# Kernel optimization log

Measured on AMD Instinct MI355X. Metric: run time of the kernel, lower is better.

The kernel has to match this reference:

```python
import jax, jax.numpy as jnp
import numpy as np

B, C, H, W = 4, 96, 256, 256
HEADS = 4
WH = WW = 8            # window size
QKV_D = C // HEADS     # qkv_dim defaults to in_channels // num_heads
N = WH * WW            # tokens per window
EPS = 1e-6


def _rel_index():
    # Swin-style relative position index, [N, N], constant
    coords = np.stack(np.meshgrid(np.arange(WH), np.arange(WW), indexing='ij'), 0).reshape(2, -1)
    rel = coords[:, :, None] - coords[:, None, :]
    rel[0] += WH - 1
    rel[1] += WW - 1
    return rel[0] * (2 * WW - 1) + rel[1]

REL = jnp.asarray(_rel_index())  # int32 [N, N]


def setup_inputs() -> dict:
    key = jax.random.key(0)
    ks = jax.random.split(key, 8)
    s = lambda k, shape: jax.random.normal(k, shape, jnp.float32) * 0.02
    return dict(
        x=jax.random.normal(ks[0], (B, C, H, W), jnp.float32),
        norm_w=jnp.ones((C,), jnp.float32),                      # RMSNorm inside MHA (channel-last tokens)
        qkv_w=s(ks[1], (3 * HEADS * QKV_D, C)),
        qkv_b=jnp.zeros((3 * HEADS * QKV_D,), jnp.float32),
        proj_w=s(ks[2], (C, HEADS * QKV_D)),
        proj_b=jnp.zeros((C,), jnp.float32),
        bias_table=s(ks[3], ((2 * WH - 1) * (2 * WW - 1),)),     # WindowScoreBias table (shared across heads)
        mlp_norm_w=jnp.ones((1, C, 1, 1), jnp.float32),          # RMSNorm1((1,C,1,1), dim=1)
        w1_w=s(ks[4], (2 * C, C, 1, 1)),                         # mid = out_channels*mlp_ratio = 2C
        w1_b=jnp.zeros((2 * C,), jnp.float32),
        w2_w=s(ks[5], (C, C, 3, 3)),                             # mid//2 = C -> C, 3x3
        w2_b=jnp.zeros((C,), jnp.float32),
    )


def rms_norm(x, w, axis):
    v = jnp.mean(x * x, axis=axis, keepdims=True)
    return x * jax.lax.rsqrt(v + EPS) * w


def conv2d(x, w, b):
    y = jax.lax.conv_general_dilated(x, w, (1, 1), 'VALID',
                                     dimension_numbers=('NCHW', 'OIHW', 'NCHW'))
    return y + b[None, :, None, None]


def reference(x, norm_w, qkv_w, qkv_b, proj_w, proj_b, bias_table,
              mlp_norm_w, w1_w, w1_b, w2_w, w2_b):
    B_, C_, H_, W_ = x.shape
    nH, nW = H_ // WH, W_ // WW
    # ---- windowed MHA with norm fused in and relative bias ----
    # window partition: [B,C,H,W] -> [B*nWin, N, C]
    xw = x.reshape(B_, C_, nH, WH, nW, WW).transpose(0, 2, 4, 3, 5, 1).reshape(-1, N, C_)
    xn = rms_norm(xw, norm_w, -1)
    qkv = xn @ qkv_w.T + qkv_b                                  # [Bn, N, 3*h*d]
    qkv = qkv.reshape(-1, N, 3, HEADS, QKV_D).transpose(2, 0, 3, 1, 4)  # [3, Bn, h, N, d]
    q, k, v = qkv[0], qkv[1], qkv[2]
    bias = bias_table[REL]                                      # [N, N], broadcast over batch/heads
    scores = jnp.einsum('bhnd,bhmd->bhnm', q, k) / jnp.sqrt(jnp.float32(QKV_D)) + bias
    attn = jax.nn.softmax(scores, axis=-1)
    o = jnp.einsum('bhnm,bhmd->bhnd', attn, v)
    o = o.transpose(0, 2, 1, 3).reshape(-1, N, HEADS * QKV_D)
    o = o @ proj_w.T + proj_b
    # reverse window partition
    o = o.reshape(B_, nH, nW, WH, WW, C_).transpose(0, 5, 1, 3, 2, 4).reshape(B_, C_, H_, W_)
    x = x + o
    # ---- GLU conv MLP residual ----
    y = rms_norm(x, mlp_norm_w, 1)
    y = conv2d(y, w1_w, w1_b)                                   # 1x1, C -> 2C
    a, g = jnp.split(y, 2, axis=1)
    y = a * jax.nn.sigmoid(g)                                   # GLU along channels
    # ReplicationPad2dDetach: edge pad whose padded ring carries no gradient
    yp = jnp.pad(jax.lax.stop_gradient(y), ((0, 0), (0, 0), (1, 1), (1, 1)), mode='edge')
    yp = yp.at[:, :, 1:-1, 1:-1].set(y)
    y = conv2d(yp, w2_w, w2_b)                                  # 3x3 valid on padded -> same size
    y = jnp.where(y >= 0, y, 0.1 * y)                           # leaky_relu(0.1)
    return x + y
```

## Files before the change

kernel.cpp:

```cpp
#include <hip/hip_runtime.h>
#include <hip/hip_bf16.h>

#define CC 96

typedef short short8  __attribute__((ext_vector_type(8)));
typedef short short4v __attribute__((ext_vector_type(4)));
typedef float f32x4   __attribute__((ext_vector_type(4)));
typedef _Float16 half4 __attribute__((ext_vector_type(4)));

#if __has_builtin(__builtin_amdgcn_mfma_f32_16x16x16_f16)
  #define MFMA16(a,b,c) __builtin_amdgcn_mfma_f32_16x16x16_f16((a),(b),(c),0,0,0)
#else
  #define MFMA16(a,b,c) __builtin_amdgcn_mfma_f32_16x16x16f16((a),(b),(c),0,0,0)
#endif

static __device__ __forceinline__ ushort f2bf(float f) {
  __hip_bfloat16 h = __float2bfloat16(f);
  return *reinterpret_cast<ushort*>(&h);
}
static __device__ __forceinline__ float bf2f(ushort u) {
  union { unsigned int u; float f; } v; v.u = ((unsigned int)u) << 16; return v.f;
}

#define QSCALE 0.20412414523193154f

__global__ void prep_kernel(const float* __restrict__ qkv_w,
                            const float* __restrict__ qkv_b,
                            const float* __restrict__ proj_w,
                            const float* __restrict__ w2w,
                            const float* __restrict__ w1w,
                            __hip_bfloat16* __restrict__ qkvp,
                            float* __restrict__ qkvb2,
                            __hip_bfloat16* __restrict__ projp,
                            __hip_bfloat16* __restrict__ w2p,
                            __hip_bfloat16* __restrict__ w1p,
                            __hip_bfloat16* __restrict__ vwp)
{
  const int i = blockIdx.x*256 + threadIdx.x;
  if (i < 36864) {
    const int e = i & 7, lane = (i >> 3) & 63;
    const int rest = i >> 9;
    const int mt = rest % 6, r2 = rest / 6;
    const int ks = r2 % 3, h = r2 / 3;
    const int od = mt*16 + (lane & 15);
    const int sec = od >> 5, d = od & 31;
    const int c = ks*32 + (lane >> 4)*8 + e;
    float val = 0.f;
    if (d < 24) {
      val = qkv_w[(sec*96 + h*24 + d)*96 + c];
      if (sec == 0) val *= QSCALE;
    }
    qkvp[i] = __float2bfloat16(val);
  }
  const int jb = i - 36864;
  if (jb >= 0 && jb < 384) {
    const int h = jb / 96, od = jb - h*96;
    const int sec = od >> 5, d = od & 31;
    float val = 0.f;
    if (d < 24) {
      val = qkv_b[sec*96 + h*24 + d];
      if (sec == 0) val *= QSCALE;
    }
    qkvb2[jb] = val;
  }
  const int j = i - 37248;
  if (j >= 0 && j < 9216) {
    const int e = j & 7, lane = (j >> 3) & 63;
    const int rest = j >> 9;
    const int nt = rest % 6, ks = rest / 6;
    const int oc = nt*16 + (lane & 15);
    const int dd = ks*32 + (lane >> 4)*8 + e;
    projp[j] = __float2bfloat16(proj_w[oc*96 + dd]);
  }
  const int k = i - 46464;
  if (k >= 0 && k < 82944) {
    const int e = k & 7;
    const int lane = (k >> 3) & 63;
    const int rest = k >> 9;
    const int nf = rest % 6;
    const int r2 = rest / 6;
    const int kc = r2 % 3;
    const int tap = r2 / 3;
    const int cidx = kc*32 + (lane >> 4)*8 + e;
    const int oc = nf*16 + (lane & 15);
    const int ky = tap / 3, kx = tap - ky*3;
    w2p[k] = __float2bfloat16(w2w[((oc*96 + cidx)*3 + ky)*3 + kx]);
  }
  const int m = i - 129408;
  if (m >= 0 && m < 18432) {
    const int e = m & 7, lane = (m >> 3) & 63;
    const int rest = m >> 9;
    const int nt = rest % 12, ks = rest / 12;
    const int oc = nt*16 + (lane & 15);
    const int c  = ks*32 + (lane >> 4)*8 + e;
    w1p[m] = __float2bfloat16(w1w[oc*96 + c]);
  }
  const int v = i - 147840;
  if (v >= 0 && v < 12288) {
    const int e = v & 7, lane = (v >> 3) & 63;
    const int rest = v >> 9;
    const int nt2 = rest % 2, r2 = rest / 2;
    const int ks = r2 % 3, h = r2 / 3;
    const int d = nt2*16 + (lane & 15);
    const int c = ks*32 + (lane >> 4)*8 + e;
    const float val = (d < 24) ? qkv_w[(192 + h*24 + d)*96 + c] : 0.f;
    vwp[v] = __float2bfloat16(val);
  }
}

__global__ __launch_bounds__(512, 2) void attn_kernel(
    const float* __restrict__ x,
    const float* __restrict__ norm_w,
    const __hip_bfloat16* __restrict__ qkvp,
    const float* __restrict__ qkvb2,
    const __hip_bfloat16* __restrict__ vwp,
    const __hip_bfloat16* __restrict__ projp,
    const float* __restrict__ proj_b,
    const float* __restrict__ bias_table,
    float* __restrict__ out)
{
  extern __shared__ char smem[];
  ushort* xn   = (ushort*)smem;
  ushort* xr   = (ushort*)(smem + 26624);
  float*  btab = (float*)(smem + 51200);

  const int wp = blockIdx.x;
  const int b   = wp >> 9;
  const int wy  = (wp >> 4) & 31;
  const int wxp = wp & 15;
  const int t  = threadIdx.x;
  const int y0 = wy*8, x0 = wxp*16;
  const int l  = t & 63;
  const int W  = __builtin_amdgcn_readfirstlane(t >> 6);
  const int w2 = W >> 2, h = W & 3;
  const int lr = l & 15, g = l >> 4;

  for (int i = t; i < 225; i += 512) btab[i] = bias_table[i];

  {
    const int p = t >> 2, q = t & 3;
    const int ty = p >> 4, tx = p & 15;
    const float* xp = x + (size_t)(b*CC + q*24)*65536 + (size_t)(y0+ty)*256 + x0 + tx;
    float xv[24]; float ss = 0.f;
    #pragma unroll
    for (int i = 0; i < 24; i++) { xv[i] = xp[(size_t)i*65536]; ss += xv[i]*xv[i]; }
    ss += __shfl_xor(ss, 1);
    ss += __shfl_xor(ss, 2);
    const float s = rsqrtf(ss * (1.f/96.f) + 1e-6f);
    const int row = (tx >> 3)*64 + ty*8 + (tx & 7);
    #pragma unroll
    for (int k2 = 0; k2 < 3; k2++) {
      short8 pk, pr;
      #pragma unroll
      for (int q2 = 0; q2 < 8; q2++) {
        pr[q2] = (short)f2bf(xv[k2*8+q2]);
        pk[q2] = (short)f2bf(xv[k2*8+q2] * s * norm_w[q*24 + k2*8 + q2]);
      }
      *(short8*)(xn + row*104 + q*24 + k2*8) = pk;
      *(short8*)(xr + row*96  + q*24 + k2*8) = pr;
    }
  }
  __syncthreads();

  half4 qf[2][4], kf[2][4];
  #pragma unroll
  for (int pass = 0; pass < 2; pass++) {
    f32x4 acc[2][4];
    #pragma unroll
    for (int m2 = 0; m2 < 2; m2++)
      #pragma unroll
      for (int nt = 0; nt < 4; nt++) acc[m2][nt] = (f32x4)0.f;
    #pragma unroll
    for (int ks = 0; ks < 3; ks++) {
      short8 bfr[4];
      #pragma unroll
      for (int nt = 0; nt < 4; nt++)
        bfr[nt] = *(const short8*)((const char*)xn + (w2*64 + nt*16 + lr)*208 + g*16 + ks*64);
      #pragma unroll
      for (int m2 = 0; m2 < 2; m2++) {
        const short8 afr = *(const short8*)(qkvp + ((h*3+ks)*6 + pass*2 + m2)*512 + l*8);
        #pragma unroll
        for (int nt = 0; nt < 4; nt++)
          acc[m2][nt] = __builtin_amdgcn_mfma_f32_16x16x32_bf16(afr, bfr[nt], acc[m2][nt], 0, 0, 0);
      }
    }
    #pragma unroll
    for (int m2 = 0; m2 < 2; m2++) {
      const f32x4 bb = *(const f32x4*)(qkvb2 + h*96 + (pass*2+m2)*16 + g*4);
      #pragma unroll
      for (int nt = 0; nt < 4; nt++)
        #pragma unroll
        for (int r = 0; r < 4; r++) {
          const float v = acc[m2][nt][r] + bb[r];
          if (pass == 0) qf[m2][nt][r] = (_Float16)v;
          else           kf[m2][nt][r] = (_Float16)v;
        }
    }
  }

  half4 pa[4][4];
  #pragma unroll
  for (int qt = 0; qt < 4; qt++) {
    f32x4 sacc[4];
    #pragma unroll
    for (int kt = 0; kt < 4; kt++) {
      f32x4 s0 = MFMA16(kf[0][kt], qf[0][qt], (f32x4)0.f);
      sacc[kt] = MFMA16(kf[1][kt], qf[1][qt], s0);
    }
    const int q = qt*16 + lr;
    const int aq = (q >> 3)*15 + (q & 7);
    float vv[4][4];
    float mx = -1e30f;
    #pragma unroll
    for (int kt = 0; kt < 4; kt++)
      #pragma unroll
      for (int r = 0; r < 4; r++) {
        const int k = kt*16 + g*4 + r;
        vv[kt][r] = sacc[kt][r] + btab[aq + 112 - ((k >> 3)*15 + (k & 7))];
        mx = fmaxf(mx, vv[kt][r]);
      }
    mx = fmaxf(mx, __shfl_xor(mx, 16));
    mx = fmaxf(mx, __shfl_xor(mx, 32));
    float sum = 0.f;
    #pragma unroll
    for (int kt = 0; kt < 4; kt++)
      #pragma unroll
      for (int r = 0; r < 4; r++) { vv[kt][r] = __expf(vv[kt][r] - mx); sum += vv[kt][r]; }
    sum += __shfl_xor(sum, 16);
    sum += __shfl_xor(sum, 32);
    const float rinv = 1.f / sum;
    #pragma unroll
    for (int kt = 0; kt < 4; kt++)
      #pragma unroll
      for (int r = 0; r < 4; r++) pa[kt][qt][r] = (_Float16)(vv[kt][r] * rinv);
  }

  half4 vb[4][2];
  {
    f32x4 vacc[4][2];
    #pragma unroll
    for (int kt = 0; kt < 4; kt++) { vacc[kt][0] = (f32x4)0.f; vacc[kt][1] = (f32x4)0.f; }
    #pragma unroll
    for (int ks = 0; ks < 3; ks++) {
      short8 afr[4];
      #pragma unroll
      for (int kt = 0; kt < 4; kt++)
        afr[kt] = *(const short8*)((const char*)xn + (w2*64 + kt*16 + lr)*208 + g*16 + ks*64);
      #pragma unroll
      for (int nt2 = 0; nt2 < 2; nt2++) {
        const short8 vwf = *(const short8*)(vwp + ((h*3+ks)*2+nt2)*512 + l*8);
        #pragma unroll
        for (int kt = 0; kt < 4; kt++)
          vacc[kt][nt2] = __builtin_amdgcn_mfma_f32_16x16x32_bf16(afr[kt], vwf, vacc[kt][nt2], 0, 0, 0);
      }
    }
    #pragma unroll
    for (int nt2 = 0; nt2 < 2; nt2++) {
      const float vbias = qkvb2[h*96 + 64 + nt2*16 + lr];
      #pragma unroll
      for (int kt = 0; kt < 4; kt++)
        #pragma unroll
        for (int r = 0; r < 4; r++)
          vb[kt][nt2][r] = (_Float16)(vacc[kt][nt2][r] + vbias);
    }
  }

  f32x4 oacc[4][2];
  #pragma unroll
  for (int qt = 0; qt < 4; qt++) { oacc[qt][0] = (f32x4)0.f; oacc[qt][1] = (f32x4)0.f; }
  #pragma unroll
  for (int kt = 0; kt < 4; kt++)
    #pragma unroll
    for (int qt = 0; qt < 4; qt++) {
      oacc[qt][0] = MFMA16(pa[kt][qt], vb[kt][0], oacc[qt][0]);
      oacc[qt][1] = MFMA16(pa[kt][qt], vb[kt][1], oacc[qt][1]);
    }
  __syncthreads();

  #pragma unroll
  for (int qt = 0; qt < 4; qt++)
    #pragma unroll
    for (int r = 0; r < 4; r++) {
      const int row = w2*64 + qt*16 + g*4 + r;
      xn[row*104 + h*24 + lr] = f2bf(oacc[qt][0][r]);
      if (lr < 8) xn[row*104 + h*24 + 16 + lr] = f2bf(oacc[qt][1][r]);
    }
  __syncthreads();

  {
    f32x4 pacc[6];
    #pragma unroll
    for (int nt = 0; nt < 6; nt++) pacc[nt] = (f32x4)0.f;
    #pragma unroll
    for (int ks = 0; ks < 3; ks++) {
      const short8 af = *(const short8*)((const char*)xn + (lr + W*16)*208 + g*16 + ks*64);
      #pragma unroll
      for (int nt = 0; nt < 6; nt++) {
        const short8 bf = *(const short8*)(projp + (ks*6+nt)*512 + l*8);
        pacc[nt] = __builtin_amdgcn_mfma_f32_16x16x32_bf16(af, bf, pacc[nt], 0, 0, 0);
      }
    }
    __syncthreads();
    ushort* oT = xn;
    #pragma unroll
    for (int nt = 0; nt < 6; nt++) {
      const int oc = lr + nt*16;
      const float bias = proj_b[oc];
      short4v pk;
      #pragma unroll
      for (int r = 0; r < 4; r++) {
        const int row = W*16 + g*4 + r;
        pk[r] = (short)f2bf(pacc[nt][r] + bias + bf2f(xr[row*96 + oc]));
      }
      *(short4v*)((char*)oT + oc*264 + (g*4 + W*16)*2) = pk;
    }
  }
  __syncthreads();

  {
    const ushort* oT = xn;
    #pragma unroll
    for (int k2 = 0; k2 < 6; k2++) {
      const int e = t + k2*512;
      const int oc = e >> 5, q5 = e & 31;
      const int ty = q5 >> 2, tq = q5 & 3;
      const int m = (tq >> 1)*64 + ty*8 + (tq & 1)*4;
      const short4v ov = *(const short4v*)((const char*)oT + oc*264 + m*2);
      const size_t gidx = (size_t)(b*CC+oc)*65536 + (size_t)(y0+ty)*256 + x0 + tq*4;
      float4 res;
      res.x = bf2f((ushort)ov[0]);
      res.y = bf2f((ushort)ov[1]);
      res.z = bf2f((ushort)ov[2]);
      res.w = bf2f((ushort)ov[3]);
      *(float4*)(out + gidx) = res;
    }
  }
}

__global__ __launch_bounds__(256, 2) void mlp1_kernel(
    const float* __restrict__ x1,
    const float* __restrict__ mlp_norm_w,
    const __hip_bfloat16* __restrict__ w1p,
    const float* __restrict__ w1_b,
    __hip_bfloat16* __restrict__ y)
{
  __shared__ ushort xn[128*104];
  const int blk = blockIdx.x;
  const int b   = blk >> 9;
  const int p0  = (blk & 511) << 7;
  const int t   = threadIdx.x;
  const int l   = t & 63;
  const int w   = __builtin_amdgcn_readfirstlane(t >> 6);
  const int lr  = l & 15, g = l >> 4;

  {
    const int p = t >> 1, half = t & 1;
    const float* xp = x1 + (size_t)(b*CC + half*48)*65536 + p0 + p;
    float xv[48];
    float ss = 0.f;
    #pragma unroll
    for (int i = 0; i < 48; i++) { xv[i] = xp[(size_t)i*65536]; ss += xv[i]*xv[i]; }
    ss += __shfl_xor(ss, 1);
    const float s = rsqrtf(ss*(1.f/96.f) + 1e-6f);
    #pragma unroll
    for (int i = 0; i < 48; i += 2) {
      const int c = half*48 + i;
      union { ushort u[2]; uint v; } pk;
      pk.u[0] = f2bf(xv[i]   * s * mlp_norm_w[c]);
      pk.u[1] = f2bf(xv[i+1] * s * mlp_norm_w[c+1]);
      *(uint*)(&xn[p*104 + c]) = pk.v;
    }
  }

  f32x4 acc[2][12];
  #pragma unroll
  for (int m2 = 0; m2 < 2; m2++)
    #pragma unroll
    for (int nt = 0; nt < 12; nt++) acc[m2][nt] = (f32x4)0.f;

  #pragma unroll
  for (int ks = 0; ks < 3; ks++) {
    short8 afr[2];
    #pragma unroll
    for (int m2 = 0; m2 < 2; m2++)
      afr[m2] = *(const short8*)((const char*)xn + (lr + (w*2+m2)*16)*208 + g*16 + ks*64);
    #pragma unroll
    for (int nt = 0; nt < 12; nt++) {
      const short8 bfr = *(const short8*)(w1p + ((ks*12+nt)*64 + l)*8);
      #pragma unroll
      for (int m2 = 0; m2 < 2; m2++)
        acc[m2][nt] = __builtin_amdgcn_mfma_f32_16x16x32_bf16(afr[m2], bfr, acc[m2][nt], 0, 0, 0);
    }
  }

  #pragma unroll
  for (int m2 = 0; m2 < 2; m2++)
    #pragma unroll
    for (int nt = 0; nt < 6; nt++) {
      const int oc = nt*16 + lr;
      const float ab = w1_b[oc], gb = w1_b[96+oc];
      #pragma unroll
      for (int r = 0; r < 4; r++) {
        const int row = (w*2+m2)*16 + g*4 + r;
        const float a  = acc[m2][nt][r]   + ab;
        const float gg = acc[m2][nt+6][r] + gb;
        xn[row*104 + oc] = f2bf(a / (1.f + __expf(-gg)));
      }
    }
  __syncthreads();

  __hip_bfloat16* yp = y + ((size_t)(b*65536 + p0))*96;
  #pragma unroll
  for (int k2 = 0; k2 < 6; k2++) {
    const int e = t + k2*256;
    const int p = e / 12, ch = e - p*12;
    const short8 v = *(const short8*)(&xn[p*104 + ch*8]);
    *(short8*)((ushort*)yp + p*96 + ch*8) = v;
  }
}

__global__ __launch_bounds__(256) void conv3_kernel(
    const __hip_bfloat16* __restrict__ y,
    const __hip_bfloat16* __restrict__ w2p,
    const float* __restrict__ w2_b,
    float* __restrict__ xout)
{
  extern __shared__ char smem[];
  ushort* A = (ushort*)smem;
  float*  O = (float*)smem;

  const int vbid = (blockIdx.x & 7)*256 + (blockIdx.x >> 3);
  const int b   = vbid >> 9;
  const int rem = vbid & 511;
  const int ch  = rem >> 7;
  const int rp  = rem & 127;
  const int px0 = ch << 6;
  const int t   = threadIdx.x;
  const int w   = __builtin_amdgcn_readfirstlane(t >> 6);
  const int l   = t & 63;
  const int m15 = l & 15, lh = l >> 4;

  for (int e = t; e < 3168; e += 256) {
    const int seg  = e / 12;
    const int part = e - seg*12;
    const int ky = seg / 66;
    const int px = seg - ky*66;
    const int gy = min(255, max(0, 2*rp + ky - 1));
    const int gx = min(255, max(0, px0 + px - 1));
    const short8 v = *(const short8*)(y + ((size_t)(b*65536 + gy*256 + gx))*96 + part*8);
    *(short8*)(A + seg*104 + part*8) = v;
  }

  f32x4 resid[12];
  #pragma unroll
  for (int k2 = 0; k2 < 12; k2++) {
    const int e = t + k2*256;
    const int oc = e >> 5;
    const int j  = (e & 31) * 4;
    const int gy = 2*rp + (j >> 6);
    const int px = px0 + (j & 63);
    resid[k2] = *(const f32x4*)(xout + ((size_t)(b*CC + oc))*65536 + (size_t)gy*256 + px);
  }
  __syncthreads();

  f32x4 acc0[6], acc1[6];
  #pragma unroll
  for (int nf = 0; nf < 6; ++nf) { acc0[nf] = (f32x4)0.f; acc1[nf] = (f32x4)0.f; }

  for (int tap = 0; tap < 9; ++tap) {
    const int ky = tap / 3, kx = tap - ky*3;
    for (int kc = 0; kc < 3; ++kc) {
      const int cb = kc*32 + lh*8;
      const short8 a0 = *(const short8*)(A + ((ky  )*66 + 16*w + m15 + kx)*104 + cb);
      const short8 a1 = *(const short8*)(A + ((ky+1)*66 + 16*w + m15 + kx)*104 + cb);
      const short8* bp = (const short8*)w2p + ((size_t)(tap*3 + kc)*6)*64 + l;
      #pragma unroll
      for (int nf = 0; nf < 6; ++nf) {
        const short8 bf = bp[nf*64];
        acc0[nf] = __builtin_amdgcn_mfma_f32_16x16x32_bf16(a0, bf, acc0[nf], 0, 0, 0);
        acc1[nf] = __builtin_amdgcn_mfma_f32_16x16x32_bf16(a1, bf, acc1[nf], 0, 0, 0);
      }
    }
  }
  __syncthreads();

  {
    const int jb = 16*w + lh*4;
    #pragma unroll
    for (int nf = 0; nf < 6; ++nf) {
      const int oc = nf*16 + m15;
      *(f32x4*)(O + oc*132 + jb)      = acc0[nf];
      *(f32x4*)(O + oc*132 + 64 + jb) = acc1[nf];
    }
  }
  __syncthreads();

  #pragma unroll
  for (int k2 = 0; k2 < 12; ++k2) {
    const int e = t + k2*256;
    const int oc = e >> 5;
    const int j  = (e & 31) * 4;
    f32x4 v = *(const f32x4*)(O + oc*132 + j);
    const float bb = w2_b[oc];
    const int gy = 2*rp + (j >> 6);
    const int px = px0 + (j & 63);
    float* op = xout + ((size_t)(b*CC + oc))*65536 + (size_t)gy*256 + px;
    f32x4 r = resid[k2];
    #pragma unroll
    for (int q = 0; q < 4; ++q) {
      float u = v[q] + bb;
      u = (u >= 0.f) ? u : 0.1f*u;
      r[q] += u;
    }
    *(f32x4*)op = r;
  }
}

extern "C" void kernel_launch(void* const* d_in, const int* in_sizes, int n_in,
                              void* d_out, int out_size, void* d_ws, size_t ws_size,
                              hipStream_t stream)
{
  (void)in_sizes; (void)n_in; (void)out_size; (void)ws_size;
  const float* x      = (const float*)d_in[0];
  const float* norm_w = (const float*)d_in[1];
  const float* qkv_w  = (const float*)d_in[2];
  const float* qkv_b  = (const float*)d_in[3];
  const float* proj_w = (const float*)d_in[4];
  const float* proj_b = (const float*)d_in[5];
  const float* btab   = (const float*)d_in[6];
  const float* mlpnw  = (const float*)d_in[7];
  const float* w1w    = (const float*)d_in[8];
  const float* w1b    = (const float*)d_in[9];
  const float* w2w    = (const float*)d_in[10];
  const float* w2b    = (const float*)d_in[11];
  float* out = (float*)d_out;

  char* ws = (char*)d_ws;
  __hip_bfloat16* y     = (__hip_bfloat16*)ws;
  __hip_bfloat16* w2p   = (__hip_bfloat16*)(ws + 50331648);
  __hip_bfloat16* qkvp  = (__hip_bfloat16*)(ws + 50497536);
  float*          qkvb2 = (float*)(ws + 50571264);
  __hip_bfloat16* projp = (__hip_bfloat16*)(ws + 50572800);
  __hip_bfloat16* w1p   = (__hip_bfloat16*)(ws + 50591232);
  __hip_bfloat16* vwp   = (__hip_bfloat16*)(ws + 50628096);

  prep_kernel<<<626, 256, 0, stream>>>(qkv_w, qkv_b, proj_w, w2w, w1w,
                                       qkvp, qkvb2, projp, w2p, w1p, vwp);

  attn_kernel<<<2048, 512, 52100, stream>>>(x, norm_w, qkvp, qkvb2, vwp, projp, proj_b, btab, out);
  mlp1_kernel<<<2048, 256, 0, stream>>>(out, mlpnw, w1p, w1b, y);
  conv3_kernel<<<2048, 256, 54912, stream>>>(y, w2p, w2b, out);
}
```

Before: 264.6 us.

## Stage conv3 weights through LDS per tap with register prefetch, write output from registers

The 3x3 conv kernel now copies each tap's weight slice into shared memory, prefetching the next tap's slice into registers while the current tap computes, instead of having every wave read weights directly from global memory. The epilogue writes results straight from the MFMA accumulators with residuals loaded in matching layout, dropping the LDS transpose and two barriers. LDS per block grows to about 73KB and launch bounds request 2 blocks per CU. This adds per-tap barriers and register pressure, and gives stores less coalescing in exchange for removing redundant global weight reads.

```diff
diff --git a/kernel.cpp b/kernel.cpp
--- a/kernel.cpp
+++ b/kernel.cpp
@@ -419,15 +419,15 @@
   }
 }
 
-__global__ __launch_bounds__(256) void conv3_kernel(
+__global__ __launch_bounds__(256, 2) void conv3_kernel(
     const __hip_bfloat16* __restrict__ y,
     const __hip_bfloat16* __restrict__ w2p,
     const float* __restrict__ w2_b,
     float* __restrict__ xout)
 {
   extern __shared__ char smem[];
-  ushort* A = (ushort*)smem;
-  float*  O = (float*)smem;
+  ushort* A  = (ushort*)smem;
+  ushort* Bs = (ushort*)(smem + 54912);
 
   const int vbid = (blockIdx.x & 7)*256 + (blockIdx.x >> 3);
   const int b   = vbid >> 9;
@@ -451,68 +451,73 @@
     *(short8*)(A + seg*104 + part*8) = v;
   }
 
-  f32x4 resid[12];
-  #pragma unroll
-  for (int k2 = 0; k2 < 12; k2++) {
-    const int e = t + k2*256;
-    const int oc = e >> 5;
-    const int j  = (e & 31) * 4;
-    const int gy = 2*rp + (j >> 6);
-    const int px = px0 + (j & 63);
-    resid[k2] = *(const f32x4*)(xout + ((size_t)(b*CC + oc))*65536 + (size_t)gy*256 + px);
-  }
-  __syncthreads();
+  f32x4 resid[2][6];
+  const int gpx = px0 + 16*w + lh*4;
+  #pragma unroll
+  for (int rw = 0; rw < 2; rw++)
+    #pragma unroll
+    for (int nf = 0; nf < 6; nf++) {
+      const int oc = nf*16 + m15;
+      resid[rw][nf] = *(const f32x4*)(xout + ((size_t)(b*CC + oc))*65536 + (size_t)(2*rp+rw)*256 + gpx);
+    }
+
+  uint2 breg[9];
+  {
+    const uint2* src = (const uint2*)w2p;
+    #pragma unroll
+    for (int i = 0; i < 9; i++) breg[i] = src[t + i*256];
+  }
 
   f32x4 acc0[6], acc1[6];
   #pragma unroll
   for (int nf = 0; nf < 6; ++nf) { acc0[nf] = (f32x4)0.f; acc1[nf] = (f32x4)0.f; }
 
   for (int tap = 0; tap < 9; ++tap) {
+    __syncthreads();
+    {
+      uint2* dst = (uint2*)Bs;
+      #pragma unroll
+      for (int i = 0; i < 9; i++) dst[t + i*256] = breg[i];
+    }
+    if (tap < 8) {
+      const uint2* src = (const uint2*)w2p + (tap+1)*2304;
+      #pragma unroll
+      for (int i = 0; i < 9; i++) breg[i] = src[t + i*256];
+    }
+    __syncthreads();
+
     const int ky = tap / 3, kx = tap - ky*3;
+    #pragma unroll
     for (int kc = 0; kc < 3; ++kc) {
       const int cb = kc*32 + lh*8;
       const short8 a0 = *(const short8*)(A + ((ky  )*66 + 16*w + m15 + kx)*104 + cb);
       const short8 a1 = *(const short8*)(A + ((ky+1)*66 + 16*w + m15 + kx)*104 + cb);
-      const short8* bp = (const short8*)w2p + ((size_t)(tap*3 + kc)*6)*64 + l;
       #pragma unroll
       for (int nf = 0; nf < 6; ++nf) {
-        const short8 bf = bp[nf*64];
+        const short8 bf = *(const short8*)(Bs + ((kc*6+nf)*64 + l)*8);
         acc0[nf] = __builtin_amdgcn_mfma_f32_16x16x32_bf16(a0, bf, acc0[nf], 0, 0, 0);
         acc1[nf] = __builtin_amdgcn_mfma_f32_16x16x32_bf16(a1, bf, acc1[nf], 0, 0, 0);
       }
     }
   }
-  __syncthreads();
-
-  {
-    const int jb = 16*w + lh*4;
-    #pragma unroll
-    for (int nf = 0; nf < 6; ++nf) {
-      const int oc = nf*16 + m15;
-      *(f32x4*)(O + oc*132 + jb)      = acc0[nf];
-      *(f32x4*)(O + oc*132 + 64 + jb) = acc1[nf];
-    }
-  }
-  __syncthreads();
-
-  #pragma unroll
-  for (int k2 = 0; k2 < 12; ++k2) {
-    const int e = t + k2*256;
-    const int oc = e >> 5;
-    const int j  = (e & 31) * 4;
-    f32x4 v = *(const f32x4*)(O + oc*132 + j);
+
+  #pragma unroll
+  for (int nf = 0; nf < 6; ++nf) {
+    const int oc = nf*16 + m15;
     const float bb = w2_b[oc];
-    const int gy = 2*rp + (j >> 6);
-    const int px = px0 + (j & 63);
-    float* op = xout + ((size_t)(b*CC + oc))*65536 + (size_t)gy*256 + px;
-    f32x4 r = resid[k2];
-    #pragma unroll
-    for (int q = 0; q < 4; ++q) {
-      float u = v[q] + bb;
-      u = (u >= 0.f) ? u : 0.1f*u;
-      r[q] += u;
-    }
-    *(f32x4*)op = r;
+    #pragma unroll
+    for (int rw = 0; rw < 2; rw++) {
+      const f32x4 av = rw ? acc1[nf] : acc0[nf];
+      float* op = xout + ((size_t)(b*CC + oc))*65536 + (size_t)(2*rp+rw)*256 + gpx;
+      f32x4 r = resid[rw][nf];
+      #pragma unroll
+      for (int q = 0; q < 4; ++q) {
+        float u = av[q] + bb;
+        u = (u >= 0.f) ? u : 0.1f*u;
+        r[q] += u;
+      }
+      *(f32x4*)op = r;
+    }
   }
 }
 
@@ -549,5 +554,5 @@
 
   attn_kernel<<<2048, 512, 52100, stream>>>(x, norm_w, qkvp, qkvb2, vwp, projp, proj_b, btab, out);
   mlp1_kernel<<<2048, 256, 0, stream>>>(out, mlpnw, w1p, w1b, y);
-  conv3_kernel<<<2048, 256, 54912, stream>>>(y, w2p, w2b, out);
-}
+  conv3_kernel<<<2048, 256, 73344, stream>>>(y, w2p, w2b, out);
+}
```

Result: faster. 232.5 us (-12.1%).
